# Optimization experiments

Hardware: AMD Instinct MI355X
Metric: run time of the kernel (lower is better)

## Reference

```python
import jax, jax.numpy as jnp
import numpy as np

B, T, D = 2, 4096, 2048
H, DH = 4, 32


def setup_inputs() -> dict:
    key = jax.random.key(0)
    k0, k1, k2, k3 = jax.random.split(key, 4)
    return {
        "hidden_states": jax.random.normal(k0, (B, T, D), dtype=jnp.float32),
        "Wq": jax.random.normal(k1, (H * DH, D), dtype=jnp.float32) * 0.02,
        "Ww": jax.random.normal(k2, (H, D), dtype=jnp.float32) * 0.02,
        "Wk": jax.random.normal(k3, (DH, D), dtype=jnp.float32) * 0.02,
    }


def reference(hidden_states, Wq, Ww, Wk):
    b, t, d = hidden_states.shape
    h, dh = Ww.shape[0], Wk.shape[0]
    # projections (nn.Linear: x @ W^T)
    q = (hidden_states @ Wq.T).reshape(b, t, h, dh)  # (B,T,H,Dh)
    w = hidden_states @ Ww.T                          # (B,T,H)
    k = hidden_states @ Wk.T                          # (B,T,Dh) shared across heads
    # multi-head QK^T -> ReLU -> per-head weighted sum (no softmax)
    raw = jnp.einsum('bthd,bsd->bths', q, k)          # (B,T,H,S)
    raw = jax.nn.relu(raw)
    index_scores = jnp.einsum('bths,bth->bts', raw, w)  # (B,T,S)
    return index_scores
```

## Files before the change

kernel.cpp:

```cpp
#include <hip/hip_runtime.h>
#include <hip/hip_bf16.h>

#define B_ 2
#define T_ 4096
#define D_ 2048
#define H_ 4
#define NC 176
#define ROWS (B_ * T_)
#define NT 11
#define TILE_E (16 * NC)
#define WTILE_E (16 * D_)

typedef __attribute__((ext_vector_type(8))) short short8;
typedef __attribute__((ext_vector_type(4))) short short4v;
typedef __attribute__((ext_vector_type(4))) float f32x4;
typedef __attribute__((ext_vector_type(4))) float float4v;

__device__ inline unsigned short f2bf(float f) {
  unsigned u = __float_as_uint(f);
  u += 0x7fffu + ((u >> 16) & 1u);
  return (unsigned short)(u >> 16);
}
__device__ inline float bf2f(unsigned short s) {
  return __uint_as_float(((unsigned)s) << 16);
}

__global__ __launch_bounds__(256) void pack_weights(const float* __restrict__ Wq,
                                                    const float* __restrict__ Ww,
                                                    const float* __restrict__ Wk,
                                                    unsigned short* __restrict__ Wcb) {
  int idx = blockIdx.x * 256 + threadIdx.x;
  if (idx >= NC * D_) return;
  int row = idx / D_, col = idx - row * D_;
  float v = 0.f;
  if (row < 128)       v = Wq[row * D_ + col];
  else if (row < 160)  v = Wk[(row - 128) * D_ + col];
  else if (row < 164)  v = Ww[(row - 160) * D_ + col];
  int n = row >> 4, r = row & 15;
  size_t dst = (size_t)n * WTILE_E + (size_t)(col >> 3) * 128 + r * 8 + (col & 7);
  Wcb[dst] = f2bf(v);
}

__global__ __launch_bounds__(256) void proj_kernel(const float* __restrict__ hs,
                                                   const unsigned short* __restrict__ Wcb,
                                                   unsigned short* __restrict__ Cb) {
  __shared__ f32x4 red[3][11][64];

  int wid  = threadIdx.x >> 6;
  int lane = threadIdx.x & 63;
  int lr = lane & 15, lo = lane >> 4;
  int row0 = blockIdx.x * 16;
  int k0   = wid * 512;

  const float*          ap    = hs  + (size_t)(row0 + lr) * D_ + k0 + lo * 8;
  const unsigned short* bbase = Wcb + (size_t)k0 * 16 + lo * 128 + lr * 8;

  f32x4 acc[11];
#pragma unroll
  for (int n = 0; n < 11; ++n) acc[n] = (f32x4){0.f, 0.f, 0.f, 0.f};

  float4v A0[2], A1[2];
  short8  Bv[2][11];

  A0[0] = *(const float4v*)(ap);
  A1[0] = *(const float4v*)(ap + 4);
#pragma unroll
  for (int n = 0; n < 11; ++n)
    Bv[0][n] = *(const short8*)(bbase + (size_t)n * WTILE_E);

#pragma unroll
  for (int s = 0; s < 16; ++s) {
    const int cur = s & 1, nxt = cur ^ 1;
    if (s < 15) {
      A0[nxt] = *(const float4v*)(ap + (s + 1) * 32);
      A1[nxt] = *(const float4v*)(ap + (s + 1) * 32 + 4);
#pragma unroll
      for (int n = 0; n < 11; ++n)
        Bv[nxt][n] = *(const short8*)(bbase + (size_t)n * WTILE_E + (s + 1) * 512);
    }
    short8 a;
#pragma unroll
    for (int i = 0; i < 4; ++i) {
      a[i]     = (short)f2bf(A0[cur][i]);
      a[i + 4] = (short)f2bf(A1[cur][i]);
    }
#pragma unroll
    for (int n = 0; n < 11; ++n)
      acc[n] = __builtin_amdgcn_mfma_f32_16x16x32_bf16(a, Bv[cur][n], acc[n], 0, 0, 0);
  }

  if (wid != 0) {
#pragma unroll
    for (int n = 0; n < 11; ++n) red[wid - 1][n][lane] = acc[n];
  }
  __syncthreads();

  if (wid == 0) {
#pragma unroll
    for (int n = 0; n < 11; ++n) {
      f32x4 r0 = red[0][n][lane], r1 = red[1][n][lane], r2 = red[2][n][lane];
#pragma unroll
      for (int r = 0; r < 4; ++r) acc[n][r] += r0[r] + r1[r] + r2[r];
    }
    unsigned short* cb = Cb + (size_t)(row0 >> 4) * TILE_E + (lr & 7);
#pragma unroll
    for (int n = 0; n < 11; ++n) {
      int oct = n * 2 + (lr >> 3);
#pragma unroll
      for (int r = 0; r < 4; ++r)
        cb[oct * 128 + (lo * 4 + r) * 8] = f2bf(acc[n][r]);
    }
  }
}

__global__ __launch_bounds__(256) void score_kernel(const unsigned short* __restrict__ Cb,
                                                    float* __restrict__ out) {
  int b = blockIdx.z, tb = blockIdx.y, sb = blockIdx.x;
  int wid  = threadIdx.x >> 6;
  int lane = threadIdx.x & 63;
  int lr = lane & 15, lo = lane >> 4;
  int wm = wid >> 1, wn = wid & 1;
  int t_base = tb * 128 + wm * 64;
  int s_base = sb * 128 + wn * 64;

  const unsigned short* C2 = Cb + (size_t)b * (T_ / 16) * TILE_E;
  float* O = out + (size_t)b * T_ * T_;

  short8 bf[4];
#pragma unroll
  for (int n = 0; n < 4; ++n)
    bf[n] = *(const short8*)(C2 + (size_t)((s_base >> 4) + n) * TILE_E +
                             (16 + lo) * 128 + lr * 8);

  const f32x4 zero = (f32x4){0.f, 0.f, 0.f, 0.f};

#pragma unroll
  for (int m = 0; m < 4; ++m) {
    const unsigned short* Ct = C2 + (size_t)((t_base >> 4) + m) * TILE_E;

    short8 af[H_];
#pragma unroll
    for (int h = 0; h < H_; ++h)
      af[h] = *(const short8*)(Ct + (h * 4 + lo) * 128 + lr * 8);

    float wv[4][H_];
    const unsigned short* wp = Ct + 20 * 128 + lo * 32;
#pragma unroll
    for (int r = 0; r < 4; ++r) {
      short4v w4 = *(const short4v*)(wp + r * 8);
#pragma unroll
      for (int h = 0; h < H_; ++h) wv[r][h] = bf2f((unsigned short)w4[h]);
    }

    int tc = t_base + m * 16 + lo * 4;
#pragma unroll
    for (int n = 0; n < 4; ++n) {
      f32x4 o = zero;
#pragma unroll
      for (int h = 0; h < H_; ++h) {
        f32x4 c = __builtin_amdgcn_mfma_f32_16x16x32_bf16(af[h], bf[n], zero, 0, 0, 0);
#pragma unroll
        for (int r = 0; r < 4; ++r) o[r] += wv[r][h] * fmaxf(c[r], 0.f);
      }
      int sc = s_base + n * 16 + lr;
#pragma unroll
      for (int r = 0; r < 4; ++r)
        O[(size_t)(tc + r) * T_ + sc] = o[r];
    }
  }
}

extern "C" void kernel_launch(void* const* d_in, const int* in_sizes, int n_in,
                              void* d_out, int out_size, void* d_ws, size_t ws_size,
                              hipStream_t stream) {
  const float* hs = (const float*)d_in[0];
  const float* Wq = (const float*)d_in[1];
  const float* Ww = (const float*)d_in[2];
  const float* Wk = (const float*)d_in[3];
  float* out = (float*)d_out;

  unsigned short* Wcb = (unsigned short*)d_ws;
  unsigned short* Cb  = (unsigned short*)((char*)d_ws + (1 << 20));

  pack_weights<<<(NC * D_ + 255) / 256, 256, 0, stream>>>(Wq, Ww, Wk, Wcb);
  proj_kernel<<<ROWS / 16, 256, 0, stream>>>(hs, Wcb, Cb);
  dim3 g(T_ / 128, T_ / 128, B_);
  score_kernel<<<g, 256, 0, stream>>>(Cb, out);
}
```

Measured before the change: 62.25 us.

## Vectorize weight packing, split projection K across 8 waves, coalesce score stores

The weight packer now has each thread load 8 floats and write one 16-byte bf16 vector, replacing scattered 2-byte stores. The projection kernel uses 512 threads, so each of 8 waves covers 256 of K. The cross-wave reduction is spread over waves in two LDS rounds instead of being done by wave 0 alone. The score kernel stages each 16x64 output tile in padded LDS and writes full rows with 16-byte nontemporal stores instead of strided scalar stores, adding LDS traffic and extra barriers in the projection.

```diff
diff --git a/kernel.cpp b/kernel.cpp
--- a/kernel.cpp
+++ b/kernel.cpp
@@ -7,7 +7,6 @@
 #define H_ 4
 #define NC 176
 #define ROWS (B_ * T_)
-#define NT 11
 #define TILE_E (16 * NC)
 #define WTILE_E (16 * D_)
 
@@ -29,28 +28,42 @@
                                                     const float* __restrict__ Ww,
                                                     const float* __restrict__ Wk,
                                                     unsigned short* __restrict__ Wcb) {
-  int idx = blockIdx.x * 256 + threadIdx.x;
-  if (idx >= NC * D_) return;
-  int row = idx / D_, col = idx - row * D_;
-  float v = 0.f;
-  if (row < 128)       v = Wq[row * D_ + col];
-  else if (row < 160)  v = Wk[(row - 128) * D_ + col];
-  else if (row < 164)  v = Ww[(row - 160) * D_ + col];
+  int row = blockIdx.x;
+  int cg  = threadIdx.x;
+  int col = cg * 8;
+
+  const float* src = nullptr;
+  if (row < 128)       src = Wq + (size_t)row * D_;
+  else if (row < 160)  src = Wk + (size_t)(row - 128) * D_;
+  else if (row < 164)  src = Ww + (size_t)(row - 160) * D_;
+
+  short8 v;
+  if (src) {
+    float4v f0 = *(const float4v*)(src + col);
+    float4v f1 = *(const float4v*)(src + col + 4);
+#pragma unroll
+    for (int i = 0; i < 4; ++i) {
+      v[i]     = (short)f2bf(f0[i]);
+      v[i + 4] = (short)f2bf(f1[i]);
+    }
+  } else {
+#pragma unroll
+    for (int i = 0; i < 8; ++i) v[i] = 0;
+  }
   int n = row >> 4, r = row & 15;
-  size_t dst = (size_t)n * WTILE_E + (size_t)(col >> 3) * 128 + r * 8 + (col & 7);
-  Wcb[dst] = f2bf(v);
-}
-
-__global__ __launch_bounds__(256) void proj_kernel(const float* __restrict__ hs,
+  *(short8*)&Wcb[(size_t)n * WTILE_E + (size_t)cg * 128 + r * 8] = v;
+}
+
+__global__ __launch_bounds__(512) void proj_kernel(const float* __restrict__ hs,
                                                    const unsigned short* __restrict__ Wcb,
                                                    unsigned short* __restrict__ Cb) {
-  __shared__ f32x4 red[3][11][64];
+  __shared__ f32x4 red[8][6][64];
 
   int wid  = threadIdx.x >> 6;
   int lane = threadIdx.x & 63;
   int lr = lane & 15, lo = lane >> 4;
   int row0 = blockIdx.x * 16;
-  int k0   = wid * 512;
+  int k0   = wid * 256;
 
   const float*          ap    = hs  + (size_t)(row0 + lr) * D_ + k0 + lo * 8;
   const unsigned short* bbase = Wcb + (size_t)k0 * 16 + lo * 128 + lr * 8;
@@ -69,9 +82,9 @@
     Bv[0][n] = *(const short8*)(bbase + (size_t)n * WTILE_E);
 
 #pragma unroll
-  for (int s = 0; s < 16; ++s) {
+  for (int s = 0; s < 8; ++s) {
     const int cur = s & 1, nxt = cur ^ 1;
-    if (s < 15) {
+    if (s < 7) {
       A0[nxt] = *(const float4v*)(ap + (s + 1) * 32);
       A1[nxt] = *(const float4v*)(ap + (s + 1) * 32 + 4);
 #pragma unroll
@@ -89,32 +102,37 @@
       acc[n] = __builtin_amdgcn_mfma_f32_16x16x32_bf16(a, Bv[cur][n], acc[n], 0, 0, 0);
   }
 
-  if (wid != 0) {
-#pragma unroll
-    for (int n = 0; n < 11; ++n) red[wid - 1][n][lane] = acc[n];
-  }
-  __syncthreads();
-
-  if (wid == 0) {
-#pragma unroll
-    for (int n = 0; n < 11; ++n) {
-      f32x4 r0 = red[0][n][lane], r1 = red[1][n][lane], r2 = red[2][n][lane];
-#pragma unroll
-      for (int r = 0; r < 4; ++r) acc[n][r] += r0[r] + r1[r] + r2[r];
-    }
-    unsigned short* cb = Cb + (size_t)(row0 >> 4) * TILE_E + (lr & 7);
-#pragma unroll
-    for (int n = 0; n < 11; ++n) {
+  unsigned short* cb = Cb + (size_t)(row0 >> 4) * TILE_E + (lr & 7);
+#pragma unroll
+  for (int g = 0; g < 2; ++g) {
+    const int ns = g * 6;
+    const int cnt = (g == 0) ? 6 : 5;
+#pragma unroll
+    for (int j = 0; j < 6; ++j)
+      if (j < cnt) red[wid][j][lane] = acc[ns + j];
+    __syncthreads();
+    if (wid < cnt) {
+      int n = ns + wid;
+      f32x4 t = red[0][wid][lane];
+#pragma unroll
+      for (int w = 1; w < 8; ++w) {
+        f32x4 p = red[w][wid][lane];
+#pragma unroll
+        for (int r = 0; r < 4; ++r) t[r] += p[r];
+      }
       int oct = n * 2 + (lr >> 3);
 #pragma unroll
       for (int r = 0; r < 4; ++r)
-        cb[oct * 128 + (lo * 4 + r) * 8] = f2bf(acc[n][r]);
-    }
+        cb[oct * 128 + (lo * 4 + r) * 8] = f2bf(t[r]);
+    }
+    __syncthreads();
   }
 }
 
 __global__ __launch_bounds__(256) void score_kernel(const unsigned short* __restrict__ Cb,
                                                     float* __restrict__ out) {
+  __shared__ __align__(16) float tbuf[4][16][76];
+
   int b = blockIdx.z, tb = blockIdx.y, sb = blockIdx.x;
   int wid  = threadIdx.x >> 6;
   int lane = threadIdx.x & 63;
@@ -133,6 +151,8 @@
                              (16 + lo) * 128 + lr * 8);
 
   const f32x4 zero = (f32x4){0.f, 0.f, 0.f, 0.f};
+  int rr = lane >> 4;
+  int cq = (lane & 15) * 4;
 
 #pragma unroll
   for (int m = 0; m < 4; ++m) {
@@ -152,7 +172,7 @@
       for (int h = 0; h < H_; ++h) wv[r][h] = bf2f((unsigned short)w4[h]);
     }
 
-    int tc = t_base + m * 16 + lo * 4;
+    f32x4 o4[4];
 #pragma unroll
     for (int n = 0; n < 4; ++n) {
       f32x4 o = zero;
@@ -162,10 +182,20 @@
 #pragma unroll
         for (int r = 0; r < 4; ++r) o[r] += wv[r][h] * fmaxf(c[r], 0.f);
       }
-      int sc = s_base + n * 16 + lr;
+      o4[n] = o;
+    }
+
+#pragma unroll
+    for (int n = 0; n < 4; ++n)
 #pragma unroll
       for (int r = 0; r < 4; ++r)
-        O[(size_t)(tc + r) * T_ + sc] = o[r];
+        tbuf[wid][lo * 4 + r][n * 16 + lr] = o4[n][r];
+
+    float* Om = O + (size_t)(t_base + m * 16) * T_ + s_base;
+#pragma unroll
+    for (int j = 0; j < 4; ++j) {
+      float4v v = *(const float4v*)&tbuf[wid][rr + 4 * j][cq];
+      __builtin_nontemporal_store(v, (float4v*)(Om + (size_t)(rr + 4 * j) * T_ + cq));
     }
   }
 }
@@ -182,8 +212,8 @@
   unsigned short* Wcb = (unsigned short*)d_ws;
   unsigned short* Cb  = (unsigned short*)((char*)d_ws + (1 << 20));
 
-  pack_weights<<<(NC * D_ + 255) / 256, 256, 0, stream>>>(Wq, Ww, Wk, Wcb);
-  proj_kernel<<<ROWS / 16, 256, 0, stream>>>(hs, Wcb, Cb);
+  pack_weights<<<NC, 256, 0, stream>>>(Wq, Ww, Wk, Wcb);
+  proj_kernel<<<ROWS / 16, 512, 0, stream>>>(hs, Wcb, Cb);
   dim3 g(T_ / 128, T_ / 128, B_);
   score_kernel<<<g, 256, 0, stream>>>(Cb, out);
 }
```

After: 64.88 us. +4.2%, slower.
